# Kernel optimization log

Hardware: AMD Instinct MI355X
Metric: run time of the kernel (lower is better)

## Reference

```python
import jax, jax.numpy as jnp
import numpy as np

NUM_FORMULAS = 256
NUM_CONJ_ARR = [6, 9, 12, 15]
DEPTH_ARR = [2, 4, 6]
TEMPERATURE = 2.0
INPUT_DIM = 512
BATCH = 8192

# --- static DNF structure (mirrors build-time indicator matrices) ---
_group = NUM_FORMULAS // len(NUM_CONJ_ARR)                       # 64 formulas per group
_conj_per_formula = np.repeat(np.array(NUM_CONJ_ARR), _group)     # [F]
_CONJ2FORM = np.repeat(np.arange(NUM_FORMULAS), _conj_per_formula)  # [C] = 2688
TOTAL_CONJ = int(_CONJ2FORM.shape[0])
_depths = np.tile(np.array(DEPTH_ARR), TOTAL_CONJ // len(DEPTH_ARR))  # depth per conjunction
_LIT2CONJ = np.repeat(np.arange(TOTAL_CONJ), _depths)             # [L] = 10752
TOTAL_LIT = int(_LIT2CONJ.shape[0])


def setup_inputs() -> dict:
    key = jax.random.key(0)
    k = jax.random.split(key, 6)
    x = jax.random.normal(k[0], (BATCH, INPUT_DIM), jnp.float32)
    # literals_random_mask: binary feature-subset mask per literal (build-time constant)
    random_mask = (jax.random.uniform(k[1], (INPUT_DIM, TOTAL_LIT)) < 0.5).astype(jnp.float32)
    glorot = jnp.sqrt(2.0 / (INPUT_DIM + TOTAL_LIT))
    # weight is pre-multiplied by the random mask at build time
    weight = jax.random.normal(k[2], (INPUT_DIM, TOTAL_LIT), jnp.float32) * glorot * random_mask
    # learnable_binary_mask: soft binary-threshold output in [0, 1]
    learnable_binary_mask = jax.random.uniform(k[3], (INPUT_DIM, TOTAL_LIT), jnp.float32)
    bias = jnp.zeros((TOTAL_LIT,), jnp.float32)
    mu = jax.random.normal(k[4], (NUM_FORMULAS, INPUT_DIM), jnp.float32)
    sigma = 1.0 + 0.1 * jax.random.uniform(k[5], (NUM_FORMULAS,), jnp.float32)
    return {
        "x": x, "weight": weight, "learnable_binary_mask": learnable_binary_mask,
        "bias": bias, "mu": mu, "sigma": sigma,
        "lit2conj": jnp.asarray(_LIT2CONJ, jnp.int32),
        "conj2form": jnp.asarray(_CONJ2FORM, jnp.int32),
    }


def reference(x, weight, learnable_binary_mask, bias, mu, sigma, lit2conj, conj2form):
    # literal projection: tanh(x @ (W * M) + b)             -> [B, L]
    literals = jnp.tanh(x @ (weight * learnable_binary_mask) + bias)
    # soft AND over literals of each conjunction: tanh(sum - d + 1.5)
    and_bias = jax.ops.segment_sum(jnp.ones((TOTAL_LIT,), literals.dtype), lit2conj,
                                   num_segments=TOTAL_CONJ)
    conj_sum = jax.ops.segment_sum(literals.T, lit2conj, num_segments=TOTAL_CONJ).T  # [B, C]
    conj = jnp.tanh(conj_sum - and_bias + 1.5)
    # soft OR over conjunctions of each formula: tanh(sum + d - 1.5)
    or_bias = jax.ops.segment_sum(jnp.ones((TOTAL_CONJ,), conj.dtype), conj2form,
                                  num_segments=NUM_FORMULAS)
    form_sum = jax.ops.segment_sum(conj.T, conj2form, num_segments=NUM_FORMULAS).T   # [B, F]
    dnnf = jnp.tanh(form_sum + or_bias - 1.5)
    # localization: softmax over formulas of temperature-scaled RBF, via GEMM expansion
    sq = (jnp.sum(x * x, axis=1, keepdims=True) - 2.0 * (x @ mu.T)
          + jnp.sum(mu * mu, axis=1)[None, :])                                       # [B, F]
    loc = jax.nn.softmax(TEMPERATURE * jnp.exp(-0.5 * sq / (sigma * sigma)[None, :]), axis=-1)
    return dnnf * loc
```

## Files before the change

kernel.cpp:

```cpp
#include <hip/hip_runtime.h>


#define BATCH 8192
#define IDIM 512
#define NFORM 256
#define NLIT 10752
#define WT_ROWS 11040

#define BM 256
#define BN 96
#define BK 64
#define LITPAD 97

typedef __bf16 bf16x8 __attribute__((ext_vector_type(8)));
typedef float f32x4 __attribute__((ext_vector_type(4)));
typedef unsigned short u16;
typedef unsigned int u32;

__device__ __forceinline__ u16 f2bf(float f) {
  u32 u = __float_as_uint(f);
  u = (u + 0x7fffu + ((u >> 16) & 1u)) >> 16;
  return (u16)u;
}

__device__ __forceinline__ float fast_tanh(float x) {
  float e = __expf(2.0f * x);
  return 1.0f - 2.0f * __builtin_amdgcn_rcpf(e + 1.0f);
}

__device__ __forceinline__ void async_cp16(const void* g, void* l) {
  __builtin_amdgcn_global_load_lds(
      (const u32 __attribute__((address_space(1)))*)g,
      (u32 __attribute__((address_space(3)))*)l, 16, 0, 0);
}


__global__ __launch_bounds__(256) void prep_x(const float* __restrict__ x,
                                              u16* __restrict__ xb,
                                              float* __restrict__ xsq) {
  int wave = threadIdx.x >> 6, lane = threadIdx.x & 63;
  int row = blockIdx.x * 4 + wave;
  const float4* px = (const float4*)(x + (size_t)row * IDIM);
  float4 a = px[lane * 2], b = px[lane * 2 + 1];
  uint4 pk;
  pk.x = (u32)f2bf(a.x) | ((u32)f2bf(a.y) << 16);
  pk.y = (u32)f2bf(a.z) | ((u32)f2bf(a.w) << 16);
  pk.z = (u32)f2bf(b.x) | ((u32)f2bf(b.y) << 16);
  pk.w = (u32)f2bf(b.z) | ((u32)f2bf(b.w) << 16);
  ((uint4*)(xb + (size_t)row * IDIM))[lane] = pk;
  float s = a.x * a.x + a.y * a.y + a.z * a.z + a.w * a.w +
            b.x * b.x + b.y * b.y + b.z * b.z + b.w * b.w;
#pragma unroll
  for (int o = 32; o > 0; o >>= 1) s += __shfl_down(s, o);
  if (lane == 0) xsq[row] = s;
}

__global__ __launch_bounds__(256) void prep_w(const float* __restrict__ W,
                                              const float* __restrict__ M,
                                              u16* __restrict__ wt) {
  __shared__ float tile[32][33];
  int l0 = blockIdx.x * 32, k0 = blockIdx.y * 32;
  int tx = threadIdx.x, ty = threadIdx.y;
#pragma unroll
  for (int i = 0; i < 4; ++i) {
    int kk = ty + i * 8;
    size_t g = (size_t)(k0 + kk) * NLIT + l0 + tx;
    tile[kk][tx] = W[g] * M[g];
  }
  __syncthreads();
#pragma unroll
  for (int i = 0; i < 4; ++i) {
    int ll = ty + i * 8;
    wt[(size_t)(l0 + ll) * IDIM + k0 + tx] = f2bf(tile[tx][ll]);
  }
}

__global__ __launch_bounds__(256) void prep_mu(const float* __restrict__ mu,
                                               u16* __restrict__ wt,
                                               float* __restrict__ musq) {
  int b = blockIdx.x, t = threadIdx.x;
  if (b < 256) {
    float s = 0.f;
#pragma unroll
    for (int j = t; j < IDIM; j += 256) {
      float v = mu[(size_t)b * IDIM + j];
      wt[(size_t)(NLIT + b) * IDIM + j] = f2bf(v);
      s += v * v;
    }
    __shared__ float red[256];
    red[t] = s;
    __syncthreads();
    for (int sh = 128; sh > 0; sh >>= 1) {
      if (t < sh) red[t] += red[t + sh];
      __syncthreads();
    }
    if (t == 0) musq[b] = red[0];
  } else {
    int row = NLIT + 256 + (b - 256);
    for (int j = t; j < IDIM; j += 256) wt[(size_t)row * IDIM + j] = 0;
  }
}


__global__ __launch_bounds__(256, 3) void dnnf_gemm(
    const u16* __restrict__ xb, const u16* __restrict__ wt,
    const float* __restrict__ bias, float* __restrict__ form_sum,
    float* __restrict__ dotbuf) {
  __shared__ __align__(16) char smraw[128 * LITPAD * 4];
  float* slit = (float*)smraw;

  const int tid = threadIdx.x;
  const int wave = tid >> 6, lane = tid & 63;
  const int m0 = blockIdx.y * BM;
  const int n0 = blockIdx.x * BN;
  const int q = lane >> 4, cn = lane & 15;

  const int kg8 = (((tid & 7) ^ ((tid >> 3) & 7))) * 8;
  const u16* pa = xb + (size_t)(m0 + (tid >> 3)) * IDIM + kg8;
  const u16* pb = wt + (size_t)(n0 + (tid >> 3)) * IDIM + kg8;
  char* dstA = smraw + tid * 16;
  char* dstB = smraw + 32768 + tid * 16;

  const int kg0_16 = ((q ^ (cn & 7)) << 4);
  int offA[4], offB[6];
#pragma unroll
  for (int mf = 0; mf < 4; ++mf)
    offA[mf] = (wave * 64 + mf * 16 + cn) * (BK * 2) + kg0_16;
#pragma unroll
  for (int nf = 0; nf < 6; ++nf)
    offB[nf] = 32768 + (nf * 16 + cn) * (BK * 2) + kg0_16;

  f32x4 acc[4][6];
#pragma unroll
  for (int a = 0; a < 4; ++a)
#pragma unroll
    for (int b = 0; b < 6; ++b) acc[a][b] = (f32x4){0.f, 0.f, 0.f, 0.f};

  for (int kt = 0; kt < IDIM; kt += BK) {
#pragma unroll
    for (int i = 0; i < 8; ++i)
      async_cp16(pa + (size_t)i * 32 * IDIM, dstA + i * 4096);
#pragma unroll
    for (int i = 0; i < 3; ++i)
      async_cp16(pb + (size_t)i * 32 * IDIM, dstB + i * 4096);
    pa += BK;
    pb += BK;
    __syncthreads();

#pragma unroll
    for (int ks = 0; ks < 2; ++ks) {
      const int x64 = ks ? 64 : 0;
      bf16x8 af[4], bfr[6];
#pragma unroll
      for (int mf = 0; mf < 4; ++mf)
        af[mf] = *(const bf16x8*)(smraw + (offA[mf] ^ x64));
#pragma unroll
      for (int nf = 0; nf < 6; ++nf)
        bfr[nf] = *(const bf16x8*)(smraw + (offB[nf] ^ x64));
#pragma unroll
      for (int mf = 0; mf < 4; ++mf)
#pragma unroll
        for (int nf = 0; nf < 6; ++nf)
          acc[mf][nf] = __builtin_amdgcn_mfma_f32_16x16x32_bf16(
              af[mf], bfr[nf], acc[mf][nf], 0, 0, 0);
    }
    __syncthreads();
  }

  if (n0 < NLIT) {
    float bv[6];
#pragma unroll
    for (int nf = 0; nf < 6; ++nf) bv[nf] = bias[n0 + nf * 16 + cn];

#pragma unroll
    for (int ph = 0; ph < 2; ++ph) {
      if (ph) __syncthreads();
      if ((wave >> 1) == ph) {
#pragma unroll
        for (int nf = 0; nf < 6; ++nf) {
          int col = nf * 16 + cn;
#pragma unroll
          for (int mf = 0; mf < 4; ++mf)
#pragma unroll
            for (int reg = 0; reg < 4; ++reg) {
              int lr = (wave & 1) * 64 + mf * 16 + q * 4 + reg;
              slit[lr * LITPAD + col] = fast_tanh(acc[mf][nf][reg] + bv[nf]);
            }
        }
      }
      __syncthreads();

      int r = tid >> 1, half = tid & 1;
      const float* lrow = slit + r * LITPAD + half * 48;
      int c0 = ((n0 + half * 48) / 12) * 3;
      size_t grow = (size_t)(m0 + ph * 128 + r) * NFORM;
      float run = 0.f;
      int fprev = -1;
#pragma unroll
      for (int tr = 0; tr < 4; ++tr) {
        const float* p = lrow + tr * 12;
        float s2 = p[0] + p[1];
        float s4 = p[2] + p[3] + p[4] + p[5];
        float s6 = p[6] + p[7] + p[8] + p[9] + p[10] + p[11];
        float v = fast_tanh(s2 - 0.5f) + fast_tanh(s4 - 2.5f) +
                  fast_tanh(s6 - 4.5f);
        int c = c0 + tr * 3;
        int f = (c < 384)    ? (c / 6)
                : (c < 960)  ? 64 + (c - 384) / 9
                : (c < 1728) ? 128 + (c - 960) / 12
                             : 192 + (c - 1728) / 15;
        if (f != fprev) {
          if (fprev >= 0) atomicAdd(form_sum + grow + fprev, run);
          fprev = f;
          run = 0.f;
        }
        run += v;
      }
      atomicAdd(form_sum + grow + fprev, run);
    }
  } else {
#pragma unroll
    for (int nf = 0; nf < 6; ++nf) {
      int col = n0 - NLIT + nf * 16 + cn;
      if (col < NFORM) {
#pragma unroll
        for (int mf = 0; mf < 4; ++mf)
#pragma unroll
          for (int reg = 0; reg < 4; ++reg) {
            int row = wave * 64 + mf * 16 + q * 4 + reg;
            dotbuf[(size_t)(m0 + row) * NFORM + col] = acc[mf][nf][reg];
          }
      }
    }
  }
}


__global__ __launch_bounds__(256) void finale(
    const float* __restrict__ form_sum, const float* __restrict__ dotbuf,
    const float* __restrict__ xsq, const float* __restrict__ musq,
    const float* __restrict__ sigma, float* __restrict__ out) {
  int wave = threadIdx.x >> 6, lane = threadIdx.x & 63;
  int r = blockIdx.x * 4 + wave;
  size_t base = (size_t)r * NFORM;
  float xs = xsq[r];
  float e[4], s = 0.f;
#pragma unroll
  for (int j = 0; j < 4; ++j) {
    int f = j * 64 + lane;
    float sq = xs - 2.0f * dotbuf[base + f] + musq[f];
    float sg = sigma[f];
    float p = __expf(-0.5f * sq / (sg * sg));
    e[j] = __expf(2.0f * p);
    s += e[j];
  }
#pragma unroll
  for (int o = 32; o > 0; o >>= 1) s += __shfl_xor(s, o);
  float inv = __builtin_amdgcn_rcpf(s);
#pragma unroll
  for (int j = 0; j < 4; ++j) {
    int f = j * 64 + lane;
    float dn = fast_tanh(form_sum[base + f] + (float)(6 + 3 * j) - 1.5f);
    out[base + f] = dn * e[j] * inv;
  }
}


extern "C" void kernel_launch(void* const* d_in, const int* in_sizes, int n_in,
                              void* d_out, int out_size, void* d_ws,
                              size_t ws_size, hipStream_t stream) {
  const float* x = (const float*)d_in[0];
  const float* W = (const float*)d_in[1];
  const float* M = (const float*)d_in[2];
  const float* bias = (const float*)d_in[3];
  const float* mu = (const float*)d_in[4];
  const float* sigma = (const float*)d_in[5];
  float* out = (float*)d_out;

  float* form_sum = (float*)d_ws;
  float* dotbuf = form_sum + (size_t)BATCH * NFORM;
  u16* xb = (u16*)(dotbuf + (size_t)BATCH * NFORM);
  u16* wt = xb + (size_t)BATCH * IDIM;
  float* xsq = (float*)(wt + (size_t)WT_ROWS * IDIM);
  float* musq = xsq + BATCH;

  hipMemsetAsync(form_sum, 0, (size_t)BATCH * NFORM * sizeof(float), stream);
  prep_x<<<BATCH / 4, 256, 0, stream>>>(x, xb, xsq);
  prep_w<<<dim3(NLIT / 32, IDIM / 32), dim3(32, 8), 0, stream>>>(W, M, wt);
  prep_mu<<<288, 256, 0, stream>>>(mu, wt, musq);
  dnnf_gemm<<<dim3(WT_ROWS / BN, BATCH / BM), 256, 0, stream>>>(xb, wt, bias,
                                                                form_sum, dotbuf);
  finale<<<BATCH / 4, 256, 0, stream>>>(form_sum, dotbuf, xsq, musq, sigma, out);
}
```

Baseline: 266.3 us.

## Double-buffer GEMM k-loop, retile to 128x192, and merge prep kernels into one launch

```diff
diff --git a/kernel.cpp b/kernel.cpp
--- a/kernel.cpp
+++ b/kernel.cpp
@@ -5,12 +5,13 @@
 #define IDIM 512
 #define NFORM 256
 #define NLIT 10752
-#define WT_ROWS 11040
-
-#define BM 256
-#define BN 96
+#define WT_ROWS 11136
+
+#define BM 128
+#define BN 192
 #define BK 64
-#define LITPAD 97
+#define BUFB 40960
+#define SLITP 196
 
 typedef __bf16 bf16x8 __attribute__((ext_vector_type(8)));
 typedef float f32x4 __attribute__((ext_vector_type(4)));
@@ -35,100 +36,114 @@
 }
 
 
-__global__ __launch_bounds__(256) void prep_x(const float* __restrict__ x,
-                                              u16* __restrict__ xb,
-                                              float* __restrict__ xsq) {
-  int wave = threadIdx.x >> 6, lane = threadIdx.x & 63;
-  int row = blockIdx.x * 4 + wave;
-  const float4* px = (const float4*)(x + (size_t)row * IDIM);
-  float4 a = px[lane * 2], b = px[lane * 2 + 1];
-  uint4 pk;
-  pk.x = (u32)f2bf(a.x) | ((u32)f2bf(a.y) << 16);
-  pk.y = (u32)f2bf(a.z) | ((u32)f2bf(a.w) << 16);
-  pk.z = (u32)f2bf(b.x) | ((u32)f2bf(b.y) << 16);
-  pk.w = (u32)f2bf(b.z) | ((u32)f2bf(b.w) << 16);
-  ((uint4*)(xb + (size_t)row * IDIM))[lane] = pk;
-  float s = a.x * a.x + a.y * a.y + a.z * a.z + a.w * a.w +
-            b.x * b.x + b.y * b.y + b.z * b.z + b.w * b.w;
-#pragma unroll
-  for (int o = 32; o > 0; o >>= 1) s += __shfl_down(s, o);
-  if (lane == 0) xsq[row] = s;
-}
-
-__global__ __launch_bounds__(256) void prep_w(const float* __restrict__ W,
-                                              const float* __restrict__ M,
-                                              u16* __restrict__ wt) {
-  __shared__ float tile[32][33];
-  int l0 = blockIdx.x * 32, k0 = blockIdx.y * 32;
-  int tx = threadIdx.x, ty = threadIdx.y;
-#pragma unroll
-  for (int i = 0; i < 4; ++i) {
-    int kk = ty + i * 8;
-    size_t g = (size_t)(k0 + kk) * NLIT + l0 + tx;
-    tile[kk][tx] = W[g] * M[g];
-  }
-  __syncthreads();
-#pragma unroll
-  for (int i = 0; i < 4; ++i) {
-    int ll = ty + i * 8;
-    wt[(size_t)(l0 + ll) * IDIM + k0 + tx] = f2bf(tile[tx][ll]);
-  }
-}
-
-__global__ __launch_bounds__(256) void prep_mu(const float* __restrict__ mu,
-                                               u16* __restrict__ wt,
-                                               float* __restrict__ musq) {
-  int b = blockIdx.x, t = threadIdx.x;
-  if (b < 256) {
-    float s = 0.f;
-#pragma unroll
-    for (int j = t; j < IDIM; j += 256) {
-      float v = mu[(size_t)b * IDIM + j];
-      wt[(size_t)(NLIT + b) * IDIM + j] = f2bf(v);
-      s += v * v;
-    }
-    __shared__ float red[256];
-    red[t] = s;
+#define PREPX_BLKS 2048
+#define PREPW_BLKS 1344
+
+__global__ __launch_bounds__(256) void prep_all(
+    const float* __restrict__ x, const float* __restrict__ W,
+    const float* __restrict__ M, const float* __restrict__ mu,
+    u16* __restrict__ xb, u16* __restrict__ wt, float* __restrict__ xsq,
+    float* __restrict__ musq, float* __restrict__ form_sum) {
+  __shared__ float lds[64 * 65];
+  const int blk = blockIdx.x, tid = threadIdx.x;
+
+  if (blk < PREPX_BLKS) {
+    ((uint4*)form_sum)[blk * 256 + tid] = make_uint4(0, 0, 0, 0);
+    int wave = tid >> 6, lane = tid & 63;
+    int row = blk * 4 + wave;
+    const float4* px = (const float4*)(x + (size_t)row * IDIM);
+    float4 a = px[lane * 2], b = px[lane * 2 + 1];
+    uint4 pk;
+    pk.x = (u32)f2bf(a.x) | ((u32)f2bf(a.y) << 16);
+    pk.y = (u32)f2bf(a.z) | ((u32)f2bf(a.w) << 16);
+    pk.z = (u32)f2bf(b.x) | ((u32)f2bf(b.y) << 16);
+    pk.w = (u32)f2bf(b.z) | ((u32)f2bf(b.w) << 16);
+    ((uint4*)(xb + (size_t)row * IDIM))[lane] = pk;
+    float s = a.x * a.x + a.y * a.y + a.z * a.z + a.w * a.w +
+              b.x * b.x + b.y * b.y + b.z * b.z + b.w * b.w;
+#pragma unroll
+    for (int o = 32; o > 0; o >>= 1) s += __shfl_down(s, o);
+    if (lane == 0) xsq[row] = s;
+  } else if (blk < PREPX_BLKS + PREPW_BLKS) {
+    int b = blk - PREPX_BLKS;
+    int l0 = (b % 168) * 64, k0 = (b / 168) * 64;
+#pragma unroll
+    for (int j = 0; j < 4; ++j) {
+      int idx = tid + j * 256;
+      int kk = idx >> 4, l4 = idx & 15;
+      size_t g = (size_t)(k0 + kk) * NLIT + l0 + l4 * 4;
+      float4 w4 = *(const float4*)(W + g);
+      float4 m4 = *(const float4*)(M + g);
+      lds[kk * 65 + l4 * 4 + 0] = w4.x * m4.x;
+      lds[kk * 65 + l4 * 4 + 1] = w4.y * m4.y;
+      lds[kk * 65 + l4 * 4 + 2] = w4.z * m4.z;
+      lds[kk * 65 + l4 * 4 + 3] = w4.w * m4.w;
+    }
     __syncthreads();
-    for (int sh = 128; sh > 0; sh >>= 1) {
-      if (t < sh) red[t] += red[t + sh];
+    int l = tid >> 2, kq = tid & 3;
+    u32 pk[8];
+#pragma unroll
+    for (int t = 0; t < 8; ++t) {
+      u16 lo = f2bf(lds[(kq * 16 + 2 * t) * 65 + l]);
+      u16 hi = f2bf(lds[(kq * 16 + 2 * t + 1) * 65 + l]);
+      pk[t] = (u32)lo | ((u32)hi << 16);
+    }
+    u32* dst = (u32*)(wt + (size_t)(l0 + l) * IDIM + k0 + kq * 16);
+    ((uint4*)dst)[0] = make_uint4(pk[0], pk[1], pk[2], pk[3]);
+    ((uint4*)dst)[1] = make_uint4(pk[4], pk[5], pk[6], pk[7]);
+  } else {
+    int b = blk - PREPX_BLKS - PREPW_BLKS;
+    if (b < 256) {
+      float s = 0.f;
+#pragma unroll
+      for (int j = tid; j < IDIM; j += 256) {
+        float v = mu[(size_t)b * IDIM + j];
+        wt[(size_t)(NLIT + b) * IDIM + j] = f2bf(v);
+        s += v * v;
+      }
+      float* red = lds;
+      red[tid] = s;
       __syncthreads();
-    }
-    if (t == 0) musq[b] = red[0];
-  } else {
-    int row = NLIT + 256 + (b - 256);
-    for (int j = t; j < IDIM; j += 256) wt[(size_t)row * IDIM + j] = 0;
-  }
-}
-
-
-__global__ __launch_bounds__(256, 3) void dnnf_gemm(
+      for (int sh = 128; sh > 0; sh >>= 1) {
+        if (tid < sh) red[tid] += red[tid + sh];
+        __syncthreads();
+      }
+      if (tid == 0) musq[b] = red[0];
+    } else {
+      int row = NLIT + 256 + (b - 256);
+      for (int j = tid; j < IDIM; j += 256) wt[(size_t)row * IDIM + j] = 0;
+    }
+  }
+}
+
+
+__global__ __launch_bounds__(256, 2) void dnnf_gemm(
     const u16* __restrict__ xb, const u16* __restrict__ wt,
     const float* __restrict__ bias, float* __restrict__ form_sum,
     float* __restrict__ dotbuf) {
-  __shared__ __align__(16) char smraw[128 * LITPAD * 4];
+  __shared__ __align__(16) char smraw[2 * BUFB];
   float* slit = (float*)smraw;
 
   const int tid = threadIdx.x;
   const int wave = tid >> 6, lane = tid & 63;
-  const int m0 = blockIdx.y * BM;
-  const int n0 = blockIdx.x * BN;
+  const int wm = wave & 1, wn = wave >> 1;
+  const int m0 = blockIdx.y * BM, n0 = blockIdx.x * BN;
   const int q = lane >> 4, cn = lane & 15;
 
-  const int kg8 = (((tid & 7) ^ ((tid >> 3) & 7))) * 8;
+  const int kg8 = ((tid & 7) ^ ((tid >> 3) & 7)) * 8;
   const u16* pa = xb + (size_t)(m0 + (tid >> 3)) * IDIM + kg8;
   const u16* pb = wt + (size_t)(n0 + (tid >> 3)) * IDIM + kg8;
-  char* dstA = smraw + tid * 16;
-  char* dstB = smraw + 32768 + tid * 16;
+  const int dA = tid * 16;
+  const int dB = 16384 + tid * 16;
 
   const int kg0_16 = ((q ^ (cn & 7)) << 4);
   int offA[4], offB[6];
 #pragma unroll
   for (int mf = 0; mf < 4; ++mf)
-    offA[mf] = (wave * 64 + mf * 16 + cn) * (BK * 2) + kg0_16;
+    offA[mf] = (wm * 64 + mf * 16 + cn) * 128 + kg0_16;
 #pragma unroll
   for (int nf = 0; nf < 6; ++nf)
-    offB[nf] = 32768 + (nf * 16 + cn) * (BK * 2) + kg0_16;
+    offB[nf] = 16384 + (wn * 96 + nf * 16 + cn) * 128 + kg0_16;
 
   f32x4 acc[4][6];
 #pragma unroll
@@ -136,27 +151,42 @@
 #pragma unroll
     for (int b = 0; b < 6; ++b) acc[a][b] = (f32x4){0.f, 0.f, 0.f, 0.f};
 
-  for (int kt = 0; kt < IDIM; kt += BK) {
-#pragma unroll
-    for (int i = 0; i < 8; ++i)
-      async_cp16(pa + (size_t)i * 32 * IDIM, dstA + i * 4096);
-#pragma unroll
-    for (int i = 0; i < 3; ++i)
-      async_cp16(pb + (size_t)i * 32 * IDIM, dstB + i * 4096);
-    pa += BK;
-    pb += BK;
-    __syncthreads();
-
+#pragma unroll
+  for (int i = 0; i < 4; ++i)
+    async_cp16(pa + (size_t)i * 32 * IDIM, smraw + dA + i * 4096);
+#pragma unroll
+  for (int i = 0; i < 6; ++i)
+    async_cp16(pb + (size_t)i * 32 * IDIM, smraw + dB + i * 4096);
+  pa += BK;
+  pb += BK;
+
+#pragma unroll
+  for (int kt = 0; kt < 8; ++kt) {
+    const char* bufc = smraw + (kt & 1) * BUFB;
+    if (kt < 7) {
+      char* bufn = smraw + ((kt + 1) & 1) * BUFB;
+#pragma unroll
+      for (int i = 0; i < 4; ++i)
+        async_cp16(pa + (size_t)i * 32 * IDIM, bufn + dA + i * 4096);
+#pragma unroll
+      for (int i = 0; i < 6; ++i)
+        async_cp16(pb + (size_t)i * 32 * IDIM, bufn + dB + i * 4096);
+      pa += BK;
+      pb += BK;
+      asm volatile("s_waitcnt vmcnt(10)\n\ts_barrier" ::: "memory");
+    } else {
+      asm volatile("s_waitcnt vmcnt(0)\n\ts_barrier" ::: "memory");
+    }
 #pragma unroll
     for (int ks = 0; ks < 2; ++ks) {
       const int x64 = ks ? 64 : 0;
       bf16x8 af[4], bfr[6];
 #pragma unroll
       for (int mf = 0; mf < 4; ++mf)
-        af[mf] = *(const bf16x8*)(smraw + (offA[mf] ^ x64));
+        af[mf] = *(const bf16x8*)(bufc + (offA[mf] ^ x64));
 #pragma unroll
       for (int nf = 0; nf < 6; ++nf)
-        bfr[nf] = *(const bf16x8*)(smraw + (offB[nf] ^ x64));
+        bfr[nf] = *(const bf16x8*)(bufc + (offB[nf] ^ x64));
 #pragma unroll
       for (int mf = 0; mf < 4; ++mf)
 #pragma unroll
@@ -164,36 +194,38 @@
           acc[mf][nf] = __builtin_amdgcn_mfma_f32_16x16x32_bf16(
               af[mf], bfr[nf], acc[mf][nf], 0, 0, 0);
     }
-    __syncthreads();
-  }
+    if (kt < 7)
+      asm volatile("s_waitcnt lgkmcnt(0)\n\ts_barrier" ::: "memory");
+  }
+  __syncthreads();
 
   if (n0 < NLIT) {
     float bv[6];
 #pragma unroll
-    for (int nf = 0; nf < 6; ++nf) bv[nf] = bias[n0 + nf * 16 + cn];
+    for (int nf = 0; nf < 6; ++nf) bv[nf] = bias[n0 + wn * 96 + nf * 16 + cn];
 
 #pragma unroll
     for (int ph = 0; ph < 2; ++ph) {
       if (ph) __syncthreads();
-      if ((wave >> 1) == ph) {
+      if (wm == ph) {
 #pragma unroll
         for (int nf = 0; nf < 6; ++nf) {
-          int col = nf * 16 + cn;
+          int col = wn * 96 + nf * 16 + cn;
 #pragma unroll
           for (int mf = 0; mf < 4; ++mf)
 #pragma unroll
             for (int reg = 0; reg < 4; ++reg) {
-              int lr = (wave & 1) * 64 + mf * 16 + q * 4 + reg;
-              slit[lr * LITPAD + col] = fast_tanh(acc[mf][nf][reg] + bv[nf]);
+              int lr = mf * 16 + q * 4 + reg;
+              slit[lr * SLITP + col] = fast_tanh(acc[mf][nf][reg] + bv[nf]);
             }
         }
       }
       __syncthreads();
 
-      int r = tid >> 1, half = tid & 1;
-      const float* lrow = slit + r * LITPAD + half * 48;
-      int c0 = ((n0 + half * 48) / 12) * 3;
-      size_t grow = (size_t)(m0 + ph * 128 + r) * NFORM;
+      int r = tid >> 2, sub = tid & 3;
+      const float* lrow = slit + r * SLITP + sub * 48;
+      int c0 = ((n0 + sub * 48) / 12) * 3;
+      size_t grow = (size_t)(m0 + ph * 64 + r) * NFORM;
       float run = 0.f;
       int fprev = -1;
 #pragma unroll
@@ -221,13 +253,13 @@
   } else {
 #pragma unroll
     for (int nf = 0; nf < 6; ++nf) {
-      int col = n0 - NLIT + nf * 16 + cn;
+      int col = n0 - NLIT + wn * 96 + nf * 16 + cn;
       if (col < NFORM) {
 #pragma unroll
         for (int mf = 0; mf < 4; ++mf)
 #pragma unroll
           for (int reg = 0; reg < 4; ++reg) {
-            int row = wave * 64 + mf * 16 + q * 4 + reg;
+            int row = wm * 64 + mf * 16 + q * 4 + reg;
             dotbuf[(size_t)(m0 + row) * NFORM + col] = acc[mf][nf][reg];
           }
       }
@@ -284,10 +316,8 @@
   float* xsq = (float*)(wt + (size_t)WT_ROWS * IDIM);
   float* musq = xsq + BATCH;
 
-  hipMemsetAsync(form_sum, 0, (size_t)BATCH * NFORM * sizeof(float), stream);
-  prep_x<<<BATCH / 4, 256, 0, stream>>>(x, xb, xsq);
-  prep_w<<<dim3(NLIT / 32, IDIM / 32), dim3(32, 8), 0, stream>>>(W, M, wt);
-  prep_mu<<<288, 256, 0, stream>>>(mu, wt, musq);
+  prep_all<<<PREPX_BLKS + PREPW_BLKS + 384, 256, 0, stream>>>(
+      x, W, M, mu, xb, wt, xsq, musq, form_sum);
   dnnf_gemm<<<dim3(WT_ROWS / BN, BATCH / BM), 256, 0, stream>>>(xb, wt, bias,
                                                                 form_sum, dotbuf);
   finale<<<BATCH / 4, 256, 0, stream>>>(form_sum, dotbuf, xsq, musq, sigma, out);
```

After: 245.2 us. 1.09x faster.
